# Optimization experiments

Measured on AMD Instinct MI355X. Metric: run time of the kernel, lower is better.

Reference implementation:

```python
import math
import jax, jax.numpy as jnp
import numpy as np

B, S, D = 2, 1024, 4096
H, DH = 32, 128


def setup_inputs() -> dict:
    key = jax.random.key(0)
    ks = jax.random.split(key, 8)
    scale = 1.0 / math.sqrt(D)
    return {
        "hidden_q": jax.random.normal(ks[0], (B, S, D), jnp.float32),
        "hidden_kv": jax.random.normal(ks[1], (B, S, D), jnp.float32),
        "attention_mask": jax.random.randint(ks[2], (B, S, S), 0, 2) > 0,
        "position_bias": jax.random.normal(ks[3], (B, H, S, S), jnp.float32),
        "Wq": jax.random.normal(ks[4], (D, H * DH), jnp.float32) * scale,
        "Wk": jax.random.normal(ks[5], (D, H * DH), jnp.float32) * scale,
        "Wv": jax.random.normal(ks[6], (D, H * DH), jnp.float32) * scale,
        "Wo": jax.random.normal(ks[7], (H * DH, D), jnp.float32) * scale,
    }


def reference(hidden_q, hidden_kv, attention_mask, position_bias, Wq, Wk, Wv, Wo):
    b, len_q, _ = hidden_q.shape
    len_k = hidden_kv.shape[1]
    # projections -> [B, H, S, DH]
    q = (hidden_q @ Wq).reshape(b, len_q, H, DH).transpose(0, 2, 1, 3)
    k = (hidden_kv @ Wk).reshape(b, len_k, H, DH).transpose(0, 2, 1, 3)
    v = (hidden_kv @ Wv).reshape(b, len_k, H, DH).transpose(0, 2, 1, 3)
    # scores [B, H, Q, K]
    score = jnp.einsum("bhqd,bhkd->bhqk", q, k) / math.sqrt(DH)
    score = score + position_bias
    mask = attention_mask[:, None, :, :]  # [B,1,Q,K]
    score = jnp.where(mask, score, -jnp.inf)
    probs = jax.nn.softmax(score, axis=-1)
    probs = jnp.where(mask, probs, 0.0)  # post-softmax mask (also kills NaN rows)
    ctx = jnp.einsum("bhqk,bhkd->bhqd", probs, v)
    ctx = ctx.transpose(0, 2, 1, 3).reshape(b, len_q, H * DH)
    out = ctx @ Wo
    return out
```

## Files before the change

kernel.cpp:

```cpp
#include <hip/hip_runtime.h>
#include <stdint.h>


#define B_  2
#define S_  1024
#define D_  4096
#define H_  32
#define DH_ 128
#define M_  (B_ * S_)
#define KSTR 8192

typedef __attribute__((ext_vector_type(8))) short bf16x8;
typedef __attribute__((ext_vector_type(4))) float f32x4;

static __device__ __forceinline__ unsigned short f32_to_bf16(float f) {
    unsigned int x = __float_as_uint(f);
    x += 0x7fffu + ((x >> 16) & 1u);
    return (unsigned short)(x >> 16);
}

static __device__ __forceinline__ f32x4 mfma16(bf16x8 a, bf16x8 b, f32x4 c) {
    return __builtin_amdgcn_mfma_f32_16x16x32_bf16(a, b, c, 0, 0, 0);
}

#if defined(__has_builtin)
#if __has_builtin(__builtin_amdgcn_global_load_lds)
#define HAVE_GLOAD_LDS 1
#endif
#endif

#ifdef HAVE_GLOAD_LDS
#define GLD16(g, lbase, lane)                                                  \
    __builtin_amdgcn_global_load_lds(                                          \
        (const __attribute__((address_space(1))) void*)(g),                    \
        (__attribute__((address_space(3))) void*)(lbase), 16, 0, 0)
#else
#define GLD16(g, lbase, lane)                                                  \
    do { *(bf16x8*)((unsigned short*)(lbase) + (size_t)(lane) * 8) =           \
             *(const bf16x8*)(g); } while (0)
#endif

__global__ void detect_mask_kernel(const unsigned char* __restrict__ m, int* flag) {
    int l = threadIdx.x;
    uint4 v = ((const uint4*)m)[l];
    unsigned int ww[4] = {v.x, v.y, v.z, v.w};
    int nz_hi = 0, nz_lo01 = 0;
#pragma unroll
    for (int wi = 0; wi < 4; ++wi)
#pragma unroll
        for (int bi = 0; bi < 4; ++bi) {
            unsigned int byte = (ww[wi] >> (bi * 8)) & 0xffu;
            if (byte && bi != 0) nz_hi = 1;
            if (byte && bi <= 1) nz_lo01 = 1;
        }
    int any_hi = __any(nz_hi);
    int any_lo01 = __any(nz_lo01);
    if (l == 0) *flag = (!any_hi) ? 1 : ((!any_lo01) ? 2 : 0);
}

__global__ void canon_mask_kernel(const void* __restrict__ m, const int* __restrict__ flag,
                                  unsigned char* __restrict__ out, int n) {
    int i = blockIdx.x * 256 + threadIdx.x;
    if (i >= n) return;
    int f = *flag;
    unsigned char v;
    if (f == 1)      v = (unsigned char)(((const int*)m)[i] != 0);
    else if (f == 2) v = (unsigned char)(((const float*)m)[i] != 0.0f);
    else             v = (unsigned char)(((const unsigned char*)m)[i] != 0);
    out[i] = v;
}

__global__ void cvt2_bf16_kernel(const float* __restrict__ a, const float* __restrict__ b,
                                 unsigned short* __restrict__ oa, unsigned short* __restrict__ ob) {
    int i = blockIdx.x * 256 + threadIdx.x;
    const int n4 = (B_ * S_ * D_) / 4;
    const float* src = (i < n4) ? a : b;
    unsigned short* dst = (i < n4) ? oa : ob;
    int j = (i < n4) ? i : i - n4;
    float4 v = ((const float4*)src)[j];
    ushort4 o;
    o.x = f32_to_bf16(v.x); o.y = f32_to_bf16(v.y);
    o.z = f32_to_bf16(v.z); o.w = f32_to_bf16(v.w);
    ((ushort4*)dst)[j] = o;
}

__global__ __launch_bounds__(256) void transpose_all_kernel(
        const float* __restrict__ Wq, const float* __restrict__ Wk,
        const float* __restrict__ Wv, const float* __restrict__ Wo,
        unsigned short* __restrict__ WTq, unsigned short* __restrict__ WTkv,
        unsigned short* __restrict__ WTo) {
    __shared__ unsigned short lds[64][65];
    int which = blockIdx.x >> 12;
    int bid = blockIdx.x & 4095;
    const float* W = (which == 0) ? Wq : (which == 1) ? Wk : (which == 2) ? Wv : Wo;
    unsigned short* WT = (which == 0) ? WTq
                       : (which == 1) ? WTkv
                       : (which == 2) ? (WTkv + (size_t)4096 * 4096)
                                      : WTo;
    int bx = bid & 63;
    int by = bid >> 6;
    int t = threadIdx.x;
    int tr = t >> 4;
    int tc = (t & 15) * 4;
#pragma unroll
    for (int p = 0; p < 4; ++p) {
        int r = p * 16 + tr;
        float4 v = *(const float4*)(W + (size_t)(by * 64 + r) * D_ + bx * 64 + tc);
        lds[r][tc + 0] = f32_to_bf16(v.x);
        lds[r][tc + 1] = f32_to_bf16(v.y);
        lds[r][tc + 2] = f32_to_bf16(v.z);
        lds[r][tc + 3] = f32_to_bf16(v.w);
    }
    __syncthreads();
#pragma unroll
    for (int p = 0; p < 4; ++p) {
        int n = p * 16 + tr;
        ushort4 o;
        o.x = lds[tc + 0][n]; o.y = lds[tc + 1][n];
        o.z = lds[tc + 2][n]; o.w = lds[tc + 3][n];
        *(ushort4*)(WT + (size_t)(bx * 64 + n) * D_ + by * 64 + tc) = o;
    }
}

__global__ __launch_bounds__(256) void vt_kernel(const unsigned short* __restrict__ KV,
                                                 unsigned short* __restrict__ Vtw) {
    __shared__ unsigned short lds[64][72];
    int bid = blockIdx.x;
    int dt = bid & 1;
    int st = (bid >> 1) & 15;
    int h  = (bid >> 5) & 31;
    int b  = bid >> 10;
    int t = threadIdx.x;
    int r = t >> 2;
    int c0 = (t & 3) * 16;
    const unsigned short* src =
        KV + (size_t)(b * S_ + st * 64 + r) * KSTR + 4096 + h * DH_ + dt * 64 + c0;
    bf16x8 v0 = *(const bf16x8*)(src);
    bf16x8 v1 = *(const bf16x8*)(src + 8);
    *(bf16x8*)&lds[r][c0] = v0;
    *(bf16x8*)&lds[r][c0 + 8] = v1;
    __syncthreads();
    unsigned short tmp[16];
#pragma unroll
    for (int i = 0; i < 16; ++i) tmp[i] = lds[c0 + i][r];
    unsigned short* dst =
        Vtw + ((size_t)((b * H_ + h) * DH_ + dt * 64 + r)) * S_ + st * 64 + c0;
    *(bf16x8*)dst = *(bf16x8*)&tmp[0];
    *(bf16x8*)(dst + 8) = *(bf16x8*)&tmp[8];
}

__device__ __forceinline__ void gemm_core(const unsigned short* __restrict__ A,
                                          const unsigned short* __restrict__ BT,
                                          void* __restrict__ C, int out_f32,
                                          int m0, int n0, int cstride,
                                          int koff, int NT, char* ldsc) {
    const int t = threadIdx.x;
    const int w = t >> 6, l = t & 63;
    const int lr = l & 15, lg = l >> 4;
    const int wmh = w >> 2;
    const int walf = w & 3;
    const int wm = wmh << 7;
    const int wn = walf << 6;

    const int ca0 = lg ^ (lr & 7);
    const int aoff0 = lr * 128 + (ca0 << 4);
    const int aoff1 = lr * 128 + ((ca0 ^ 4) << 4);
    const int boff0 = ((walf & 1) * 64 + lr) * 128 + (ca0 << 4);
    const int boff1 = ((walf & 1) * 64 + lr) * 128 + ((ca0 ^ 4) << 4);

    const int srow = t >> 3;
    const int sch = (t & 7) ^ (srow & 7);
    const size_t soff0 = (size_t)srow * 4096 + (size_t)(sch << 3);
    const size_t soff1 = soff0 + (size_t)64 * 4096;
    const int ldso = w << 10;

    f32x4 ac[8][4];
    f32x4 vzero = {0.f, 0.f, 0.f, 0.f};
#pragma unroll
    for (int i = 0; i < 8; ++i)
#pragma unroll
        for (int j = 0; j < 4; ++j) ac[i][j] = vzero;

#define STAGE_ELEM(E, SS)                                                      \
    do {                                                                       \
        int er_ = (E) & 3;                                                     \
        const unsigned short* mb_ = (er_ < 2)                                  \
            ? A + (size_t)(m0 + ((er_ & 1) << 7)) * 4096                       \
            : BT + (size_t)(n0 + ((er_ & 1) << 7)) * 4096;                     \
        mb_ += (size_t)((((E) >> 2) << 6) + koff);                             \
        char* d0_ = ldsc + (SS) * 16384 + ldso;                                \
        GLD16(mb_ + soff0, d0_, l);                                            \
        GLD16(mb_ + soff1, d0_ + 8192, l);                                     \
    } while (0)

#pragma unroll
    for (int e = 0; e < 5; ++e) STAGE_ELEM(e, e);

    const int NT4 = NT << 2;
    int E = 5, ss = 5, s0 = 0;
    bf16x8 bfr[4][2];

#pragma unroll 1
    for (int tau = 0; tau < NT; ++tau) {
        int sA = s0 + wmh;          if (sA >= 9) sA -= 9;
        int sB = s0 + 2 + (walf >> 1); if (sB >= 9) sB -= 9;
        const char* pA0 = ldsc + sA * 16384 + aoff0;
        const char* pA1 = ldsc + sA * 16384 + aoff1;
        const char* pB0 = ldsc + sB * 16384 + boff0;
        const char* pB1 = ldsc + sB * 16384 + boff1;
#pragma unroll
        for (int r = 0; r < 4; ++r) {
            if (r == 0) {
                if (tau == NT - 1)
                    asm volatile("s_waitcnt vmcnt(0)" ::: "memory");
                else
                    asm volatile("s_waitcnt vmcnt(2)" ::: "memory");
            }
            __builtin_amdgcn_s_barrier();
            asm volatile("" ::: "memory");
            if (r == 0) {
#pragma unroll
                for (int nf = 0; nf < 4; ++nf) {
                    bfr[nf][0] = *(const bf16x8*)(pB0 + nf * 2048);
                    bfr[nf][1] = *(const bf16x8*)(pB1 + nf * 2048);
                }
            }
            bf16x8 af[2][2];
            int mfb = r << 1;
#pragma unroll
            for (int j = 0; j < 2; ++j) {
                af[j][0] = *(const bf16x8*)(pA0 + (mfb + j) * 2048);
                af[j][1] = *(const bf16x8*)(pA1 + (mfb + j) * 2048);
            }
            if (E < NT4) STAGE_ELEM(E, ss);
            ++E; ss = (ss == 8) ? 0 : ss + 1;
            __builtin_amdgcn_s_setprio(1);
#pragma unroll
            for (int j = 0; j < 2; ++j)
#pragma unroll
                for (int nf = 0; nf < 4; ++nf) {
                    ac[mfb + j][nf] = mfma16(af[j][0], bfr[nf][0], ac[mfb + j][nf]);
                    ac[mfb + j][nf] = mfma16(af[j][1], bfr[nf][1], ac[mfb + j][nf]);
                }
            __builtin_amdgcn_s_setprio(0);
        }
        s0 += 4; if (s0 >= 9) s0 -= 9;
    }
#undef STAGE_ELEM

#pragma unroll
    for (int mf = 0; mf < 8; ++mf)
#pragma unroll
        for (int nf = 0; nf < 4; ++nf)
#pragma unroll
            for (int q = 0; q < 4; ++q) {
                int row = m0 + wm + mf * 16 + lg * 4 + q;
                int col = n0 + wn + nf * 16 + lr;
                if (out_f32)
                    ((float*)C)[(size_t)row * cstride + col] = ac[mf][nf][q];
                else
                    ((unsigned short*)C)[(size_t)row * cstride + col] = f32_to_bf16(ac[mf][nf][q]);
            }
}

__global__ __launch_bounds__(512, 2) void gemm_qkv_kernel(
        const unsigned short* __restrict__ Aq, const unsigned short* __restrict__ Bq,
        float* __restrict__ Pq,
        const unsigned short* __restrict__ Akv, const unsigned short* __restrict__ Bkv,
        unsigned short* __restrict__ Ckv) {
    __shared__ char ldsbuf[9 * 16384];
    int bid = blockIdx.x;
    if (bid < 256) {
        int bm = bid & 7, bn = bid >> 3;
        gemm_core(Akv, Bkv, Ckv, 0, bm << 8, bn << 8, 8192, 0, 64, ldsbuf);
    } else {
        int e = bid - 256;
        int bm = e & 7;
        int rest = e >> 3;
        int bn = rest & 15;
        int ks = rest >> 4;
        gemm_core(Aq, Bq, Pq + (size_t)ks * M_ * D_, 1, bm << 8, bn << 8, 4096,
                  ks * 2048, 32, ldsbuf);
    }
}

__global__ void reduce_q_kernel(const float* __restrict__ P, unsigned short* __restrict__ out) {
    int i = blockIdx.x * 256 + threadIdx.x;
    float4 a = ((const float4*)P)[i];
    float4 b = ((const float4*)(P + (size_t)M_ * D_))[i];
    ushort4 o;
    o.x = f32_to_bf16(a.x + b.x); o.y = f32_to_bf16(a.y + b.y);
    o.z = f32_to_bf16(a.z + b.z); o.w = f32_to_bf16(a.w + b.w);
    ((ushort4*)out)[i] = o;
}

__global__ __launch_bounds__(512, 2) void gemm_o_kernel(
        const unsigned short* __restrict__ A, const unsigned short* __restrict__ BT,
        float* __restrict__ P) {
    __shared__ char ldsbuf[9 * 16384];
    int bid = blockIdx.x;
    int bm = bid & 7;
    int rest = bid >> 3;
    int bn = rest & 15;
    int ks = rest >> 4;
    gemm_core(A, BT, P + (size_t)ks * M_ * D_, 1, bm << 8, bn << 8, 4096,
              ks * 2048, 32, ldsbuf);
}

__global__ void reduce_o_kernel(const float* __restrict__ P, float* __restrict__ out) {
    int i = blockIdx.x * 256 + threadIdx.x;
    float4 a = ((const float4*)P)[i];
    float4 b = ((const float4*)(P + (size_t)M_ * D_))[i];
    float4 o; o.x = a.x + b.x; o.y = a.y + b.y; o.z = a.z + b.z; o.w = a.w + b.w;
    ((float4*)out)[i] = o;
}

#define NEGF (-1e30f)
__global__ __launch_bounds__(256, 2) void attn_kernel(const unsigned short* __restrict__ Qw,
                                                      const unsigned short* __restrict__ KV,
                                                      const unsigned short* __restrict__ Vtw,
                                                      const float* __restrict__ bias,
                                                      const unsigned char* __restrict__ maskc,
                                                      unsigned short* __restrict__ ctx) {
    __shared__ unsigned short Kbuf[2][64 * 128];
    __shared__ unsigned short Vbuf[2][128 * 64];
    __shared__ unsigned short Plds[4][16 * 72];

    int bid = blockIdx.x;
    int qt = bid & 15, h = (bid >> 4) & 31, b = bid >> 9;
    int t = threadIdx.x, w = t >> 6, l = t & 63;
    int lr = l & 15, lg = l >> 4;
    int q0 = (qt << 6) + (w << 4);

    bf16x8 qf[4];
    const unsigned short* Qp = Qw + ((size_t)(b * S_ + q0 + lr)) * D_ + h * DH_ + lg * 8;
#pragma unroll
    for (int kf = 0; kf < 4; ++kf) qf[kf] = *(const bf16x8*)(Qp + kf * 32);

    f32x4 o[8];
    f32x4 vzero = {0.f, 0.f, 0.f, 0.f};
#pragma unroll
    for (int i = 0; i < 8; ++i) o[i] = vzero;
    float m_run[4], l_run[4];
#pragma unroll
    for (int r = 0; r < 4; ++r) { m_run[r] = NEGF; l_run[r] = 0.f; }

    const float* biasp = bias + (((size_t)(b * H_ + h)) << 20)
                              + (((size_t)(q0 + (lg << 2))) << 10) + lr;
    const unsigned char* mp = maskc + ((size_t)b << 20)
                              + (((size_t)(q0 + (lg << 2))) << 10) + lr;
    const unsigned short* Kg = KV + (size_t)(b * S_) * KSTR + h * DH_;
    const unsigned short* Vg = Vtw + (((size_t)(b * H_ + h)) * DH_) * S_;

    float br0[16], br1[16];
    int mr0[16], mr1[16];

#define STAGE_KV(KT, BUF)                                                          \
    do { int kv0_ = (KT) << 6;                                                     \
        _Pragma("unroll")                                                          \
        for (int c = 0; c < 4; ++c) {                                              \
            int seg = (w << 2) + c;                                                \
            int krow = (seg << 2) + (l >> 4);                                      \
            int kch = (l & 15) ^ (krow & 7);                                       \
            GLD16(Kg + (size_t)(kv0_ + krow) * KSTR + (kch << 3),                  \
                  &Kbuf[BUF][seg << 9], l);                                        \
            int vrow = (seg << 3) + (l >> 3);                                      \
            int vch = (l & 7) ^ (vrow & 7);                                        \
            GLD16(Vg + (size_t)vrow * S_ + kv0_ + (vch << 3),                      \
                  &Vbuf[BUF][seg << 9], l);                                        \
        }                                                                          \
    } while (0)

#define LOAD_BM(BR, MR, KT)                                                        \
    do { int kv0_ = (KT) << 6;                                                     \
        _Pragma("unroll")                                                          \
        for (int nb = 0; nb < 4; ++nb)                                             \
            _Pragma("unroll")                                                      \
            for (int r = 0; r < 4; ++r) {                                          \
                BR[nb * 4 + r] = biasp[((size_t)r << 10) + kv0_ + (nb << 4)];      \
                MR[nb * 4 + r] = mp[((size_t)r << 10) + kv0_ + (nb << 4)];         \
            }                                                                      \
    } while (0)

#define COMPUTE(BUF, BR, MR)                                                       \
    do {                                                                           \
        f32x4 s_[4];                                                               \
        _Pragma("unroll")                                                          \
        for (int nb = 0; nb < 4; ++nb) {                                           \
            s_[nb] = vzero;                                                        \
            int krow = (nb << 4) + lr;                                             \
            _Pragma("unroll")                                                      \
            for (int kf = 0; kf < 4; ++kf) {                                       \
                int ba = ((krow << 8) + (((kf << 5) + (lg << 3)) << 1))            \
                         ^ ((krow & 7) << 4);                                      \
                bf16x8 kfr = *(const bf16x8*)((const char*)Kbuf[BUF] + ba);        \
                s_[nb] = mfma16(qf[kf], kfr, s_[nb]);                              \
            }                                                                      \
        }                                                                          \
        float sv[4][4];                                                            \
        _Pragma("unroll")                                                          \
        for (int nb = 0; nb < 4; ++nb)                                             \
            _Pragma("unroll")                                                      \
            for (int r = 0; r < 4; ++r) {                                          \
                float x = fmaf(s_[nb][r], 0.08838834764831845f, BR[nb * 4 + r]);   \
                sv[nb][r] = MR[nb * 4 + r] ? x : NEGF;                             \
            }                                                                      \
        float mt[4], al[4], rs[4];                                                 \
        _Pragma("unroll")                                                          \
        for (int r = 0; r < 4; ++r)                                                \
            mt[r] = fmaxf(fmaxf(sv[0][r], sv[1][r]), fmaxf(sv[2][r], sv[3][r]));   \
        _Pragma("unroll")                                                          \
        for (int off = 1; off < 16; off <<= 1)                                     \
            _Pragma("unroll")                                                      \
            for (int r = 0; r < 4; ++r) mt[r] = fmaxf(mt[r], __shfl_xor(mt[r], off, 64)); \
        _Pragma("unroll")                                                          \
        for (int r = 0; r < 4; ++r) {                                              \
            float mn = fmaxf(m_run[r], mt[r]);                                     \
            al[r] = __expf(m_run[r] - mn);                                         \
            m_run[r] = mn;                                                         \
        }                                                                          \
        _Pragma("unroll")                                                          \
        for (int nb = 0; nb < 4; ++nb)                                             \
            _Pragma("unroll")                                                      \
            for (int r = 0; r < 4; ++r) sv[nb][r] = __expf(sv[nb][r] - m_run[r]);  \
        _Pragma("unroll")                                                          \
        for (int r = 0; r < 4; ++r)                                                \
            rs[r] = (sv[0][r] + sv[1][r]) + (sv[2][r] + sv[3][r]);                 \
        _Pragma("unroll")                                                          \
        for (int off = 1; off < 16; off <<= 1)                                     \
            _Pragma("unroll")                                                      \
            for (int r = 0; r < 4; ++r) rs[r] += __shfl_xor(rs[r], off, 64);       \
        _Pragma("unroll")                                                          \
        for (int r = 0; r < 4; ++r) l_run[r] = l_run[r] * al[r] + rs[r];           \
        _Pragma("unroll")                                                          \
        for (int nb2 = 0; nb2 < 8; ++nb2) {                                        \
            o[nb2][0] *= al[0]; o[nb2][1] *= al[1];                                \
            o[nb2][2] *= al[2]; o[nb2][3] *= al[3];                                \
        }                                                                          \
        _Pragma("unroll")                                                          \
        for (int nb = 0; nb < 4; ++nb)                                             \
            _Pragma("unroll")                                                      \
            for (int r = 0; r < 4; ++r)                                            \
                Plds[w][((lg << 2) + r) * 72 + (nb << 4) + lr] = f32_to_bf16(sv[nb][r]); \
        _Pragma("unroll")                                                          \
        for (int kf2 = 0; kf2 < 2; ++kf2) {                                        \
            bf16x8 pf = *(const bf16x8*)&Plds[w][lr * 72 + (kf2 << 5) + (lg << 3)]; \
            _Pragma("unroll")                                                      \
            for (int nb2 = 0; nb2 < 8; ++nb2) {                                    \
                int dh = (nb2 << 4) + lr;                                          \
                int ba = ((dh << 7) + (((kf2 << 5) + (lg << 3)) << 1))             \
                         ^ ((dh & 7) << 4);                                        \
                bf16x8 vf = *(const bf16x8*)((const char*)Vbuf[BUF] + ba);         \
                o[nb2] = mfma16(pf, vf, o[nb2]);                                   \
            }                                                                      \
        }                                                                          \
    } while (0)

    STAGE_KV(0, 0);
    LOAD_BM(br0, mr0, 0);

#pragma unroll 1
    for (int kt = 0; kt < 16; kt += 2) {
        __syncthreads();
        STAGE_KV(kt + 1, 1);
        LOAD_BM(br1, mr1, kt + 1);
        COMPUTE(0, br0, mr0);
        __syncthreads();
        if (kt < 14) {
            STAGE_KV(kt + 2, 0);
            LOAD_BM(br0, mr0, kt + 2);
        }
        COMPUTE(1, br1, mr1);
    }

#pragma unroll
    for (int r = 0; r < 4; ++r) {
        float inv = l_run[r] > 0.f ? 1.0f / l_run[r] : 0.f;
        int q = q0 + (lg << 2) + r;
        unsigned short* cp = ctx + ((size_t)(b * S_ + q)) * D_ + h * DH_ + lr;
#pragma unroll
        for (int nb2 = 0; nb2 < 8; ++nb2)
            cp[nb2 * 16] = f32_to_bf16(o[nb2][r] * inv);
    }
#undef STAGE_KV
#undef LOAD_BM
#undef COMPUTE
}

extern "C" void kernel_launch(void* const* d_in, const int* in_sizes, int n_in,
                              void* d_out, int out_size, void* d_ws, size_t ws_size,
                              hipStream_t stream) {
    const float* hq   = (const float*)d_in[0];
    const float* hkv  = (const float*)d_in[1];
    const void*  mask = d_in[2];
    const float* bias = (const float*)d_in[3];
    const float* Wq   = (const float*)d_in[4];
    const float* Wk   = (const float*)d_in[5];
    const float* Wv   = (const float*)d_in[6];
    const float* Wo   = (const float*)d_in[7];
    float* out = (float*)d_out;

    char* ws = (char*)d_ws;
    unsigned char* mask_c = (unsigned char*)ws;
    int* flag             = (int*)(ws + (2u << 20));
    unsigned short* hq_b  = (unsigned short*)(ws + (2u << 20) + 4096);
    unsigned short* hkv_b = hq_b + ((size_t)1 << 23);
    unsigned short* WTq   = hkv_b + ((size_t)1 << 23);
    unsigned short* WTo   = WTq + ((size_t)1 << 24);
    unsigned short* WTkv  = WTo + ((size_t)1 << 24);
    unsigned short* Qws   = WTkv + ((size_t)1 << 25);
    unsigned short* KVws  = Qws + ((size_t)1 << 23);
    unsigned short* Cws   = KVws + ((size_t)1 << 24);
    unsigned short* Vtw   = Cws + ((size_t)1 << 23);
    float* Pws            = (float*)(Vtw + ((size_t)1 << 23));

    detect_mask_kernel<<<1, 64, 0, stream>>>((const unsigned char*)mask, flag);
    canon_mask_kernel<<<8192, 256, 0, stream>>>(mask, flag, mask_c, B_ * S_ * S_);
    cvt2_bf16_kernel<<<16384, 256, 0, stream>>>(hq, hkv, hq_b, hkv_b);
    transpose_all_kernel<<<16384, 256, 0, stream>>>(Wq, Wk, Wv, Wo, WTq, WTkv, WTo);

    gemm_qkv_kernel<<<512, 512, 0, stream>>>(hq_b, WTq, Pws, hkv_b, WTkv, KVws);
    reduce_q_kernel<<<(M_ * D_) / 1024, 256, 0, stream>>>(Pws, Qws);

    vt_kernel<<<B_ * H_ * 16 * 2, 256, 0, stream>>>(KVws, Vtw);
    attn_kernel<<<B_ * H_ * (S_ / 64), 256, 0, stream>>>(Qws, KVws, Vtw, bias, mask_c, Cws);

    gemm_o_kernel<<<256, 512, 0, stream>>>(Cws, WTo, Pws);
    reduce_o_kernel<<<(M_ * D_) / 1024, 256, 0, stream>>>(Pws, out);
}
```

Baseline: 508.6 us.

## Transpose QK^T MFMA so each lane owns one query row; vectorize bias/mask loads

Swaps the MFMA operand order for the score tile so each lane holds four consecutive key columns of a single query row. Bias and mask can then be read as one float4 and one packed 32-bit word per block instead of scalar gathers, and row max and sum need only two cross-lane shuffles instead of four per row. The rescale factors and final normalizers are broadcast back to the output layout with __shfl, and the P tile is written to LDS in the transposed layout. s_setprio hints are added around the MFMA sections to favour matrix issue. The cost is extra broadcast shuffles and a changed LDS write pattern that could cause bank conflicts.

```diff
diff --git a/kernel.cpp b/kernel.cpp
--- a/kernel.cpp
+++ b/kernel.cpp
@@ -341,19 +341,17 @@
     f32x4 vzero = {0.f, 0.f, 0.f, 0.f};
 #pragma unroll
     for (int i = 0; i < 8; ++i) o[i] = vzero;
-    float m_run[4], l_run[4];
-#pragma unroll
-    for (int r = 0; r < 4; ++r) { m_run[r] = NEGF; l_run[r] = 0.f; }
+    float m_run = NEGF, l_run = 0.f;
 
     const float* biasp = bias + (((size_t)(b * H_ + h)) << 20)
-                              + (((size_t)(q0 + (lg << 2))) << 10) + lr;
+                              + (((size_t)(q0 + lr)) << 10);
     const unsigned char* mp = maskc + ((size_t)b << 20)
-                              + (((size_t)(q0 + (lg << 2))) << 10) + lr;
+                              + (((size_t)(q0 + lr)) << 10);
     const unsigned short* Kg = KV + (size_t)(b * S_) * KSTR + h * DH_;
     const unsigned short* Vg = Vtw + (((size_t)(b * H_ + h)) * DH_) * S_;
 
-    float br0[16], br1[16];
-    int mr0[16], mr1[16];
+    float4 br0[4], br1[4];
+    unsigned int mr0[4], mr1[4];
 
 #define STAGE_KV(KT, BUF)                                                          \
     do { int kv0_ = (KT) << 6;                                                     \
@@ -374,17 +372,16 @@
 #define LOAD_BM(BR, MR, KT)                                                        \
     do { int kv0_ = (KT) << 6;                                                     \
         _Pragma("unroll")                                                          \
-        for (int nb = 0; nb < 4; ++nb)                                             \
-            _Pragma("unroll")                                                      \
-            for (int r = 0; r < 4; ++r) {                                          \
-                BR[nb * 4 + r] = biasp[((size_t)r << 10) + kv0_ + (nb << 4)];      \
-                MR[nb * 4 + r] = mp[((size_t)r << 10) + kv0_ + (nb << 4)];         \
-            }                                                                      \
+        for (int nb = 0; nb < 4; ++nb) {                                           \
+            BR[nb] = *(const float4*)(biasp + kv0_ + (nb << 4) + (lg << 2));       \
+            MR[nb] = *(const unsigned int*)(mp + kv0_ + (nb << 4) + (lg << 2));    \
+        }                                                                          \
     } while (0)
 
 #define COMPUTE(BUF, BR, MR)                                                       \
     do {                                                                           \
         f32x4 s_[4];                                                               \
+        __builtin_amdgcn_s_setprio(1);                                             \
         _Pragma("unroll")                                                          \
         for (int nb = 0; nb < 4; ++nb) {                                           \
             s_[nb] = vzero;                                                        \
@@ -394,54 +391,58 @@
                 int ba = ((krow << 8) + (((kf << 5) + (lg << 3)) << 1))            \
                          ^ ((krow & 7) << 4);                                      \
                 bf16x8 kfr = *(const bf16x8*)((const char*)Kbuf[BUF] + ba);        \
-                s_[nb] = mfma16(qf[kf], kfr, s_[nb]);                              \
+                s_[nb] = mfma16(kfr, qf[kf], s_[nb]);    \
             }                                                                      \
         }                                                                          \
+        __builtin_amdgcn_s_setprio(0);                                             \
         float sv[4][4];                                                            \
+        _Pragma("unroll")                                                          \
+        for (int nb = 0; nb < 4; ++nb) {                                           \
+            float bb[4] = {BR[nb].x, BR[nb].y, BR[nb].z, BR[nb].w};                \
+            _Pragma("unroll")                                                      \
+            for (int r = 0; r < 4; ++r) {                                          \
+                float x = fmaf(s_[nb][r], 0.08838834764831845f, bb[r]);            \
+                sv[nb][r] = ((MR[nb] >> (r * 8)) & 0xffu) ? x : NEGF;              \
+            }                                                                      \
+        }                                                                          \
+                         \
+        float mt = sv[0][0];                                                       \
+        _Pragma("unroll")                                                          \
+        for (int nb = 0; nb < 4; ++nb)                                             \
+            _Pragma("unroll")                                                      \
+            for (int r = 0; r < 4; ++r) mt = fmaxf(mt, sv[nb][r]);                 \
+        mt = fmaxf(mt, __shfl_xor(mt, 16, 64));                                    \
+        mt = fmaxf(mt, __shfl_xor(mt, 32, 64));                                    \
+        float mn = fmaxf(m_run, mt);                                               \
+        float al = __expf(m_run - mn);                                             \
+        m_run = mn;                                                                \
+        float rs = 0.f;                                                            \
         _Pragma("unroll")                                                          \
         for (int nb = 0; nb < 4; ++nb)                                             \
             _Pragma("unroll")                                                      \
             for (int r = 0; r < 4; ++r) {                                          \
-                float x = fmaf(s_[nb][r], 0.08838834764831845f, BR[nb * 4 + r]);   \
-                sv[nb][r] = MR[nb * 4 + r] ? x : NEGF;                             \
+                sv[nb][r] = __expf(sv[nb][r] - m_run);                             \
+                rs += sv[nb][r];                                                   \
             }                                                                      \
-        float mt[4], al[4], rs[4];                                                 \
-        _Pragma("unroll")                                                          \
-        for (int r = 0; r < 4; ++r)                                                \
-            mt[r] = fmaxf(fmaxf(sv[0][r], sv[1][r]), fmaxf(sv[2][r], sv[3][r]));   \
-        _Pragma("unroll")                                                          \
-        for (int off = 1; off < 16; off <<= 1)                                     \
-            _Pragma("unroll")                                                      \
-            for (int r = 0; r < 4; ++r) mt[r] = fmaxf(mt[r], __shfl_xor(mt[r], off, 64)); \
-        _Pragma("unroll")                                                          \
-        for (int r = 0; r < 4; ++r) {                                              \
-            float mn = fmaxf(m_run[r], mt[r]);                                     \
-            al[r] = __expf(m_run[r] - mn);                                         \
-            m_run[r] = mn;                                                         \
+        rs += __shfl_xor(rs, 16, 64);                                              \
+        rs += __shfl_xor(rs, 32, 64);                                              \
+        l_run = l_run * al + rs;                                                   \
+         \
+        float alm[4];                                                              \
+        _Pragma("unroll")                                                          \
+        for (int r = 0; r < 4; ++r) alm[r] = __shfl(al, (lg << 2) + r, 64);        \
+        _Pragma("unroll")                                                          \
+        for (int nb2 = 0; nb2 < 8; ++nb2) {                                        \
+            o[nb2][0] *= alm[0]; o[nb2][1] *= alm[1];                              \
+            o[nb2][2] *= alm[2]; o[nb2][3] *= alm[3];                              \
         }                                                                          \
-        _Pragma("unroll")                                                          \
-        for (int nb = 0; nb < 4; ++nb)                                             \
-            _Pragma("unroll")                                                      \
-            for (int r = 0; r < 4; ++r) sv[nb][r] = __expf(sv[nb][r] - m_run[r]);  \
-        _Pragma("unroll")                                                          \
-        for (int r = 0; r < 4; ++r)                                                \
-            rs[r] = (sv[0][r] + sv[1][r]) + (sv[2][r] + sv[3][r]);                 \
-        _Pragma("unroll")                                                          \
-        for (int off = 1; off < 16; off <<= 1)                                     \
-            _Pragma("unroll")                                                      \
-            for (int r = 0; r < 4; ++r) rs[r] += __shfl_xor(rs[r], off, 64);       \
-        _Pragma("unroll")                                                          \
-        for (int r = 0; r < 4; ++r) l_run[r] = l_run[r] * al[r] + rs[r];           \
-        _Pragma("unroll")                                                          \
-        for (int nb2 = 0; nb2 < 8; ++nb2) {                                        \
-            o[nb2][0] *= al[0]; o[nb2][1] *= al[1];                                \
-            o[nb2][2] *= al[2]; o[nb2][3] *= al[3];                                \
-        }                                                                          \
+                                     \
         _Pragma("unroll")                                                          \
         for (int nb = 0; nb < 4; ++nb)                                             \
             _Pragma("unroll")                                                      \
             for (int r = 0; r < 4; ++r)                                            \
-                Plds[w][((lg << 2) + r) * 72 + (nb << 4) + lr] = f32_to_bf16(sv[nb][r]); \
+                Plds[w][lr * 72 + (nb << 4) + (lg << 2) + r] = f32_to_bf16(sv[nb][r]); \
+        __builtin_amdgcn_s_setprio(1);                                             \
         _Pragma("unroll")                                                          \
         for (int kf2 = 0; kf2 < 2; ++kf2) {                                        \
             bf16x8 pf = *(const bf16x8*)&Plds[w][lr * 72 + (kf2 << 5) + (lg << 3)]; \
@@ -454,6 +455,7 @@
                 o[nb2] = mfma16(pf, vf, o[nb2]);                                   \
             }                                                                      \
         }                                                                          \
+        __builtin_amdgcn_s_setprio(0);                                             \
     } while (0)
 
     STAGE_KV(0, 0);
@@ -473,9 +475,12 @@
         COMPUTE(1, br1, mr1);
     }
 
+    float lm[4];
+#pragma unroll
+    for (int r = 0; r < 4; ++r) lm[r] = __shfl(l_run, (lg << 2) + r, 64);
 #pragma unroll
     for (int r = 0; r < 4; ++r) {
-        float inv = l_run[r] > 0.f ? 1.0f / l_run[r] : 0.f;
+        float inv = lm[r] > 0.f ? 1.0f / lm[r] : 0.f;
         int q = q0 + (lg << 2) + r;
         unsigned short* cp = ctx + ((size_t)(b * S_ + q)) * D_ + h * DH_ + lr;
 #pragma unroll
```

New measurement: 504.8 us. Within noise of the previous version (-0.7%).
